# Optimization experiments

Hardware: AMD Instinct MI355X
Metric: run time of the kernel (lower is better)

## Reference

```python
import jax, jax.numpy as jnp
import numpy as np

B, L, ENC = 128, 196, 512
E, D, A, V = 512, 512, 512, 10000
MAXLEN = 26


def setup_inputs() -> dict:
    key = jax.random.key(0)
    ks = jax.random.split(key, 24)
    f32 = jnp.float32
    def rn(k, shape, scale=0.02):
        return jax.random.normal(k, shape, f32) * scale
    lengths = jax.random.randint(ks[2], (B,), 2, MAXLEN + 1).at[0].set(MAXLEN)
    return {
        'encoder_out': jax.random.normal(ks[0], (B, L, ENC), f32),
        'captions': jax.random.randint(ks[1], (B, MAXLEN), 0, V),
        'caption_lengths': lengths,
        # embedding and output layer: uniform(-0.1, 0.1) per _init_weights
        'emb': jax.random.uniform(ks[3], (V, E), f32, -0.1, 0.1),
        'W_ih': rn(ks[4], (E, 4 * D)), 'W_hh': rn(ks[5], (D, 4 * D)),
        'b_lstm': jnp.zeros((4 * D,), f32),
        # sentinel gate of AdaptiveLSTMCell
        'Wx_s': rn(ks[6], (E, D)), 'Wh_s': rn(ks[7], (D, D)), 'b_s': jnp.zeros((D,), f32),
        # adaptive attention MLP
        'W_v': rn(ks[8], (ENC, A)), 'b_v': jnp.zeros((A,), f32),
        'W_g': rn(ks[9], (D, A)), 'b_g': jnp.zeros((A,), f32),
        'W_s_att': rn(ks[10], (ENC, A)), 'b_sa': jnp.zeros((A,), f32),
        'w_a': rn(ks[11], (A,)),
        # hidden-state init layers
        'W_init_h': rn(ks[12], (ENC, D)), 'b_init_h': jnp.zeros((D,), f32),
        'W_init_c': rn(ks[13], (ENC, D)), 'b_init_c': jnp.zeros((D,), f32),
        # deep output layer
        'W_Lh': rn(ks[14], (D, E)), 'b_Lh': jnp.zeros((E,), f32),
        'W_Lz': rn(ks[15], (ENC, E)), 'b_Lz': jnp.zeros((E,), f32),
        'W_Lo': jax.random.uniform(ks[16], (E, V), f32, -0.1, 0.1),
        'b_Lo': jnp.zeros((V,), f32),
    }


def reference(encoder_out, captions, caption_lengths, emb, W_ih, W_hh, b_lstm,
              Wx_s, Wh_s, b_s, W_v, b_v, W_g, b_g, W_s_att, b_sa, w_a,
              W_init_h, b_init_h, W_init_c, b_init_c, W_Lh, b_Lh, W_Lz, b_Lz,
              W_Lo, b_Lo):
    T = captions.shape[1] - 1  # static max decode length (lengths max == MAXLEN)
    mean_ann = encoder_out.mean(axis=1)                       # (B, ENC)
    h0 = jnp.tanh(mean_ann @ W_init_h + b_init_h)             # (B, D)
    c0 = jnp.tanh(mean_ann @ W_init_c + b_init_c)
    att_v = encoder_out @ W_v + b_v                           # (B, L, A), hoisted out of the loop

    def step(carry, words):
        h, c = carry
        x = emb[words]                                        # (B, E) embedding gather
        gates = x @ W_ih + h @ W_hh + b_lstm                  # (B, 4D)
        i, f, g, o = jnp.split(gates, 4, axis=-1)
        c_new = jax.nn.sigmoid(f) * c + jax.nn.sigmoid(i) * jnp.tanh(g)
        h_new = jax.nn.sigmoid(o) * jnp.tanh(c_new)
        s_gate = jax.nn.sigmoid(x @ Wx_s + h @ Wh_s + b_s)    # sentinel (input) gate
        s = s_gate * jnp.tanh(c_new)                          # visual sentinel
        ag = h_new @ W_g + b_g                                # (B, A)
        e_v = jnp.tanh(att_v + ag[:, None, :]) @ w_a          # (B, L)
        e_s = jnp.tanh(s @ W_s_att + b_sa + ag) @ w_a         # (B,)
        a_hat = jax.nn.softmax(jnp.concatenate([e_v, e_s[:, None]], axis=1), axis=1)
        alpha, beta = a_hat[:, :-1], a_hat[:, -1]             # (B,L), (B,)
        ctx = jnp.einsum('bl,ble->be', alpha, encoder_out) + beta[:, None] * s
        logits = (x + h_new @ W_Lh + b_Lh + ctx @ W_Lz + b_Lz) @ W_Lo + b_Lo
        return (h_new, c_new), (logits, alpha, beta)

    words_t = captions[:, :T].T                               # (T, B)
    _, (preds, alphas, betas) = jax.lax.scan(step, (h0, c0), words_t)
    preds = preds.transpose(1, 0, 2)                          # (B, T, V)
    alphas = alphas.transpose(1, 0, 2)                        # (B, T, L)
    betas = betas.T                                           # (B, T)
    dec_len = jnp.clip(caption_lengths - 1, 1)
    active = (jnp.arange(T)[None, :] < dec_len[:, None]).astype(preds.dtype)
    return preds, alphas * active[:, :, None], betas * active
```

## Files before the change

kernel.cpp:

```cpp
#include <hip/hip_runtime.h>
#include <hip/hip_bf16.h>
#include <cstdint>
#include <cstddef>

using bf16 = __hip_bfloat16;
typedef __attribute__((ext_vector_type(4))) float f32x4;
typedef __attribute__((ext_vector_type(8))) short bf16x8;

#define B_ 128
#define L_ 196
#define T_ 25
#define V_ 10000
#define ESCL 2.885390081777927f

__device__ __forceinline__ float b2f(short s) {
  unsigned u = ((unsigned)(unsigned short)s) << 16;
  return __uint_as_float(u);
}
__device__ __forceinline__ bf16 f2b(float f) { return __float2bfloat16(f); }
__device__ __forceinline__ short f2bs(float f) {
  return __builtin_bit_cast(short, __float2bfloat16(f));
}
__device__ __forceinline__ float sigf(float x) { return 1.f / (1.f + __expf(-x)); }
__device__ __forceinline__ float tanh_fast(float x) { return 1.f - 2.f / (1.f + __expf(2.f * x)); }

__device__ __forceinline__ void cst_u32(unsigned* p, unsigned v) {
  __hip_atomic_store(p, v, __ATOMIC_RELAXED, __HIP_MEMORY_SCOPE_AGENT);
}
__device__ __forceinline__ unsigned cld_u32(const unsigned* p) {
  return __hip_atomic_load((unsigned*)p, __ATOMIC_RELAXED, __HIP_MEMORY_SCOPE_AGENT);
}

__device__ __forceinline__ size_t pidx(int row, int col, int K) {
  int KT = K >> 5;
  return (((size_t)(row >> 4) * KT + (col >> 5)) * 64 +
          (size_t)(((col & 31) >> 3) * 16 + (row & 15))) * 8 + (col & 7);
}

__device__ __forceinline__ float wred_sum(float x) {
#pragma unroll
  for (int off = 32; off >= 1; off >>= 1) x += __shfl_xor(x, off, 64);
  return x;
}
__device__ __forceinline__ float wred_max(float x) {
#pragma unroll
  for (int off = 32; off >= 1; off >>= 1) x = fmaxf(x, __shfl_xor(x, off, 64));
  return x;
}

__device__ __forceinline__ void gbar32(unsigned* bs, int mi, int di) {
  asm volatile("s_waitcnt vmcnt(0)" ::: "memory");
  __syncthreads();
  if (threadIdx.x == 0) {
    unsigned* base = bs + mi * 256;
    unsigned* gen  = base + 160;
    unsigned g = cld_u32(gen);
    unsigned a = __hip_atomic_fetch_add(base + (di & 3) * 32, 1u, __ATOMIC_RELAXED,
                                        __HIP_MEMORY_SCOPE_AGENT);
    bool rel = false;
    if ((a & 7u) == 7u) {
      unsigned b = __hip_atomic_fetch_add(base + 128, 1u, __ATOMIC_RELAXED,
                                          __HIP_MEMORY_SCOPE_AGENT);
      if ((b & 3u) == 3u) { cst_u32(gen, g + 1u); rel = true; }
    }
    if (!rel) {
      while (cld_u32(gen) == g) __builtin_amdgcn_s_sleep(1);
    }
  }
  __syncthreads();
}

__global__ __launch_bounds__(256) void scan_ws(
    bf16* __restrict__ hbuf,
    const bf16* __restrict__ WT_gh,
    const bf16* __restrict__ xg,
    float* __restrict__ cbuf,
    bf16* __restrict__ Aag,
    bf16* __restrict__ projA,
    unsigned* __restrict__ bar)
{
  const int tid = threadIdx.x;
  const int wv = tid >> 6, lane = tid & 63;
  const int mi = blockIdx.x >> 5;
  const int di = blockIdx.x & 31;
  __shared__ f32x4 pacc[4][5][64];

  bf16x8 bw[5][4];
#pragma unroll
  for (int g = 0; g < 5; g++)
#pragma unroll
    for (int kk = 0; kk < 4; kk++)
      bw[g][kk] = *(const bf16x8*)(const void*)(
          WT_gh + (size_t)(g * 32 + di) * 8192 + (size_t)(wv * 4 + kk) * 512 + lane * 8);

  const int el_r16 = lane & 15, el_r = lane >> 4;
  const int m_pw = mi * 16 + wv * 4 + el_r;
  const int d_pw = di * 16 + el_r16;
  const size_t qlo = pidx(m_pw, d_pw, 512);
  const size_t plo = pidx(m_pw, d_pw, 1024);
  const size_t phi = pidx(m_pw, 512 + d_pw, 1024);
  float* cp = cbuf + m_pw * 512 + d_pw;

  for (int tt = 0; tt < T_; ++tt) {
    const short* xr = (const short*)(const void*)(
        xg + (size_t)tt * (128 * 2560) + (size_t)m_pw * 2560 + d_pw);
    float xv0 = b2f(xr[0]);
    float xv1 = b2f(xr[512]);
    float xv2 = b2f(xr[1024]);
    float xv3 = b2f(xr[1536]);
    float xv4 = b2f(xr[2048]);
    const bf16* ap = hbuf + (size_t)tt * 65536 + (size_t)mi * 8192 + lane * 8;
    bf16x8 a0 = *(const bf16x8*)(const void*)(ap + (size_t)(wv * 4 + 0) * 512);
    bf16x8 a1 = *(const bf16x8*)(const void*)(ap + (size_t)(wv * 4 + 1) * 512);
    bf16x8 a2 = *(const bf16x8*)(const void*)(ap + (size_t)(wv * 4 + 2) * 512);
    bf16x8 a3 = *(const bf16x8*)(const void*)(ap + (size_t)(wv * 4 + 3) * 512);
    f32x4 acc[5];
#pragma unroll
    for (int g = 0; g < 5; g++) acc[g] = f32x4{0.f, 0.f, 0.f, 0.f};
#pragma unroll
    for (int g = 0; g < 5; g++) {
      acc[g] = __builtin_amdgcn_mfma_f32_16x16x32_bf16(a0, bw[g][0], acc[g], 0, 0, 0);
      acc[g] = __builtin_amdgcn_mfma_f32_16x16x32_bf16(a1, bw[g][1], acc[g], 0, 0, 0);
      acc[g] = __builtin_amdgcn_mfma_f32_16x16x32_bf16(a2, bw[g][2], acc[g], 0, 0, 0);
      acc[g] = __builtin_amdgcn_mfma_f32_16x16x32_bf16(a3, bw[g][3], acc[g], 0, 0, 0);
    }
#pragma unroll
    for (int g = 0; g < 5; g++) pacc[wv][g][lane] = acc[g];
    __syncthreads();
    float G0 = 0.f, G1 = 0.f, G2 = 0.f, G3 = 0.f, G4 = 0.f;
#pragma unroll
    for (int q = 0; q < 4; q++) {
      int sl = wv * 16 + el_r16;
      G0 += pacc[q][0][sl][el_r];
      G1 += pacc[q][1][sl][el_r];
      G2 += pacc[q][2][sl][el_r];
      G3 += pacc[q][3][sl][el_r];
      G4 += pacc[q][4][sl][el_r];
    }
    float cn = sigf(G1 + xv1) * (*cp) + sigf(G0 + xv0) * tanh_fast(G2 + xv2);
    float tcn = tanh_fast(cn);
    float hn = sigf(G3 + xv3) * tcn;
    float ss = sigf(G4 + xv4) * tcn;
    float hn1 = __shfl_down(hn, 1);
    float ss1 = __shfl_down(ss, 1);
    unsigned hp = 0, sp = 0;
    bool wr = !(el_r16 & 1);
    if (wr) {
      hp = (unsigned)(unsigned short)f2bs(hn) |
           ((unsigned)(unsigned short)f2bs(hn1) << 16);
      sp = (unsigned)(unsigned short)f2bs(ss) |
           ((unsigned)(unsigned short)f2bs(ss1) << 16);
      cst_u32((unsigned*)(void*)(hbuf + (size_t)(tt + 1) * 65536 + qlo), hp);
    }
    if (tt < T_ - 1) gbar32(bar, mi, di);
    *cp = cn;
    if (wr) {
      bf16* pA = projA + (size_t)tt * 131072;
      bf16* AagT = Aag + (size_t)tt * 131072;
      *(unsigned*)(void*)(pA + plo) = hp;
      *(unsigned*)(void*)(AagT + plo) = hp;
      *(unsigned*)(void*)(AagT + phi) = sp;
    }
  }
}

__global__ __launch_bounds__(256) void e_batch(
    const bf16* __restrict__ attv, const bf16* __restrict__ agsw_all,
    const float* __restrict__ w_a, const int* __restrict__ clen,
    float* __restrict__ alphas, float* __restrict__ betas,
    float* __restrict__ alphas_raw, float* __restrict__ betas_raw)
{
  __shared__ float sh[200];
  __shared__ float red[8];
  int b = blockIdx.x, t = blockIdx.y;
  int tid = threadIdx.x, wv = tid >> 6, lane = tid & 63;
  const bf16* ag = agsw_all + ((size_t)t * 128 + b) * 1024;
  int a0 = lane * 8;
  float ag8[8], wa8[8], sw8[8];
  float wsum = 0.f;
  bf16x8 agv = *(const bf16x8*)(const void*)(ag + a0);
  bf16x8 swv = *(const bf16x8*)(const void*)(ag + 512 + a0);
#pragma unroll
  for (int j = 0; j < 8; j++) {
    ag8[j] = b2f(agv[j]);
    wa8[j] = w_a[a0 + j];
    sw8[j] = b2f(swv[j]);
    wsum += wa8[j];
  }
  wsum = wred_sum(wsum);
  for (int base = wv; base < 197; base += 16) {
    bf16x8 av[4];
#pragma unroll
    for (int q = 0; q < 4; q++) {
      int l = base + 4 * q;
      if (l < 196)
        av[q] = *(const bf16x8*)(const void*)(attv + ((size_t)(b * 196 + l)) * 512 + a0);
    }
#pragma unroll
    for (int q = 0; q < 4; q++) {
      int l = base + 4 * q;
      if (l > 196) continue;
      float part = 0.f;
      if (l < 196) {
#pragma unroll
        for (int j = 0; j < 8; j++) {
          float z = b2f(av[q][j]) + ag8[j];
          float E = __builtin_amdgcn_exp2f(z);
          part = fmaf(wa8[j], __builtin_amdgcn_rcpf(1.f + E), part);
        }
      } else {
#pragma unroll
        for (int j = 0; j < 8; j++) {
          float z = sw8[j] + ag8[j];
          float E = __builtin_amdgcn_exp2f(z);
          part = fmaf(wa8[j], __builtin_amdgcn_rcpf(1.f + E), part);
        }
      }
      part = wred_sum(part);
      if (lane == 0) sh[l] = wsum - 2.f * part;
    }
  }
  __syncthreads();
  float v = (tid < 197) ? sh[tid] : -1e30f;
  float mx = wred_max(v);
  if (lane == 0) red[wv] = mx;
  __syncthreads();
  mx = fmaxf(fmaxf(red[0], red[1]), fmaxf(red[2], red[3]));
  float p = (tid < 197) ? __expf(v - mx) : 0.f;
  float sm = wred_sum(p);
  if (lane == 0) red[4 + wv] = sm;
  __syncthreads();
  float inv = 1.f / (red[4] + red[5] + red[6] + red[7]);
  float a = p * inv;
  int dec = clen[b] - 1; if (dec < 1) dec = 1;
  float act = (t < dec) ? 1.f : 0.f;
  if (tid < 196) {
    alphas[(size_t)b * (T_ * L_) + (size_t)t * L_ + tid] = a * act;
    alphas_raw[(size_t)b * (T_ * L_) + (size_t)t * L_ + tid] = a;
  }
  if (tid == 196) {
    betas[b * T_ + t] = a * act;
    betas_raw[b * T_ + t] = a;
  }
}

__global__ __launch_bounds__(256) void ctx_tail(
    const float* __restrict__ alphas_raw, const float* __restrict__ betas_raw,
    const bf16* __restrict__ enc_r, const bf16* __restrict__ Aag,
    bf16* __restrict__ projA)
{
  int b = blockIdx.x, cs = blockIdx.y, tid = threadIdx.x;
  __shared__ float al[T_ * 200];
  for (int i = tid; i < T_ * 196; i += 256) {
    al[(i / 196) * 200 + (i % 196)] = alphas_raw[(size_t)b * (T_ * 196) + i];
  }
  __syncthreads();
  int ch = cs * 256 + tid;
  float acc[T_];
#pragma unroll
  for (int t = 0; t < T_; t++) acc[t] = 0.f;
  const short* ep = (const short*)(const void*)(enc_r) + (size_t)b * 196 * 512 + ch;
#pragma unroll 4
  for (int l = 0; l < 196; l++) {
    float e = b2f(ep[(size_t)l * 512]);
#pragma unroll
    for (int t = 0; t < T_; t++) acc[t] += al[t * 200 + l] * e;
  }
#pragma unroll
  for (int t = 0; t < T_; t++) {
    float beta = betas_raw[b * T_ + t];
    float sv = b2f(((const short*)(const void*)Aag)[(size_t)t * 131072 + pidx(b, 512 + ch, 1024)]);
    projA[(size_t)t * 131072 + pidx(b, 512 + ch, 1024)] = f2b(acc[t] + beta * sv);
  }
}

enum { EPI_F32 = 0, EPI_BF16 = 1, EPI_INIT = 2, EPI_PROJ = 3, EPI_OUT = 4 };

template<int MFRAG, int NFRAG, int EPI>
__global__ __launch_bounds__(256) void gemm_pk(
    const bf16* __restrict__ A, const bf16* __restrict__ BT,
    const float* __restrict__ bias, void* __restrict__ Cp,
    const bf16* __restrict__ auxA, float* __restrict__ auxB,
    int M, int N, int K, int ldc, float oscale)
{
  const int lane = threadIdx.x & 63;
  const int wv = threadIdx.x >> 6;
  const int r16 = lane & 15;
  const int kg = lane >> 4;
  const int m0 = blockIdx.x * (MFRAG * 16);
  const int n0 = blockIdx.y * (NFRAG * 64) + wv * (NFRAG * 16);
  const int KT = K >> 5;

  f32x4 acc[MFRAG][NFRAG];
#pragma unroll
  for (int i = 0; i < MFRAG; i++)
#pragma unroll
    for (int j = 0; j < NFRAG; j++) acc[i][j] = f32x4{0.f, 0.f, 0.f, 0.f};

  const bf16* ap = A + (size_t)(m0 >> 4) * KT * 512 + lane * 8;
  const bf16* bp = BT + (size_t)(n0 >> 4) * KT * 512 + lane * 8;

#pragma unroll 4
  for (int kt = 0; kt < KT; kt++) {
    bf16x8 af[MFRAG], bfr[NFRAG];
#pragma unroll
    for (int i = 0; i < MFRAG; i++)
      af[i] = *(const bf16x8*)(const void*)(ap + ((size_t)i * KT + kt) * 512);
#pragma unroll
    for (int j = 0; j < NFRAG; j++)
      bfr[j] = *(const bf16x8*)(const void*)(bp + ((size_t)j * KT + kt) * 512);
#pragma unroll
    for (int i = 0; i < MFRAG; i++)
#pragma unroll
      for (int j = 0; j < NFRAG; j++)
        acc[i][j] = __builtin_amdgcn_mfma_f32_16x16x32_bf16(af[i], bfr[j], acc[i][j], 0, 0, 0);
  }

#pragma unroll
  for (int i = 0; i < MFRAG; i++)
#pragma unroll
    for (int j = 0; j < NFRAG; j++)
#pragma unroll
      for (int r = 0; r < 4; r++) {
        int m = m0 + i * 16 + kg * 4 + r;
        int n = n0 + j * 16 + r16;
        if (n >= N) continue;
        float v = acc[i][j][r] + bias[n];
        if constexpr (EPI == EPI_F32) {
          ((float*)Cp)[(size_t)m * ldc + n] = v * oscale;
        } else if constexpr (EPI == EPI_BF16) {
          ((bf16*)Cp)[(size_t)m * ldc + n] = f2b(v * oscale);
        } else if constexpr (EPI == EPI_INIT) {
          float tv = tanhf(v);
          if (n < 512) ((bf16*)Cp)[pidx(m, n, 512)] = f2b(tv);
          else auxB[(size_t)m * 512 + (n - 512)] = tv;
        } else if constexpr (EPI == EPI_PROJ) {
          v += b2f(((const short*)auxA)[pidx(m, n, 512)]);
          ((bf16*)Cp)[pidx(m, n, 512)] = f2b(v);
        } else {
          int t = m >> 7, b = m & 127;
          ((float*)Cp)[(size_t)b * (T_ * V_) + (size_t)t * V_ + n] = v;
        }
      }
}

#define NJOBS 10
struct TJobs {
  const float* top[NJOBS];
  const float* bot[NJOBS];
  bf16* dst[NJOBS];
  int ncols[NJOBS];
  int ktop[NJOBS];
  int K[NJOBS];
  long cum[NJOBS + 1];
};

__global__ void trans_pack_multi(TJobs J, long total)
{
  for (long u = (long)blockIdx.x * blockDim.x + threadIdx.x; u < total;
       u += (long)gridDim.x * blockDim.x) {
    int j = 0;
#pragma unroll
    for (int q = 1; q < NJOBS; q++) j += (u >= J.cum[q]) ? 1 : 0;
    long t8 = u - J.cum[j];
    int K = J.K[j], KT = K >> 5, ktop = J.ktop[j], ncols = J.ncols[j];
    const float* top = J.top[j];
    const float* bot = J.bot[j];
    int r = (int)(t8 & 15);
    int kg = (int)((t8 >> 4) & 3);
    long tile = t8 >> 6;
    int kt = (int)(tile % KT);
    int rt = (int)(tile / KT);
    int n = rt * 16 + r;
    int kb = kt * 32 + kg * 8;
    bf16x8 out;
#pragma unroll
    for (int jj = 0; jj < 8; jj++) {
      int k = kb + jj;
      float v = 0.f;
      if (n < ncols) {
        if (k < ktop) { if (top) v = top[(size_t)k * ncols + n]; }
        else if (bot) { v = bot[(size_t)(k - ktop) * ncols + n]; }
      }
      out[jj] = f2bs(v);
    }
    *(bf16x8*)(void*)(J.dst[j] + t8 * 8) = out;
  }
}

__global__ void trans_pack(const float* __restrict__ top, const float* __restrict__ bot,
                           bf16* __restrict__ dst, int ncols, long nElem8, int ktop, int K)
{
  int KT = K >> 5;
  for (long t8 = (long)blockIdx.x * blockDim.x + threadIdx.x; t8 < nElem8;
       t8 += (long)gridDim.x * blockDim.x) {
    int r = (int)(t8 & 15);
    int kg = (int)((t8 >> 4) & 3);
    long tile = t8 >> 6;
    int kt = (int)(tile % KT);
    int rt = (int)(tile / KT);
    int n = rt * 16 + r;
    int kb = kt * 32 + kg * 8;
    bf16x8 out;
#pragma unroll
    for (int j = 0; j < 8; j++) {
      int k = kb + j;
      float v = 0.f;
      if (n < ncols) {
        if (k < ktop) { if (top) v = top[(size_t)k * ncols + n]; }
        else if (bot) { v = bot[(size_t)(k - ktop) * ncols + n]; }
      }
      out[j] = f2bs(v);
    }
    *(bf16x8*)(void*)(dst + t8 * 8) = out;
  }
}

__global__ void conv_pack(const float* __restrict__ src, bf16* __restrict__ dst,
                          bf16* __restrict__ dst_row, long nElem8)
{
  for (long t8 = (long)blockIdx.x * blockDim.x + threadIdx.x; t8 < nElem8;
       t8 += (long)gridDim.x * blockDim.x) {
    int r = (int)(t8 & 15);
    int kg = (int)((t8 >> 4) & 3);
    long tile = t8 >> 6;
    int kt = (int)(tile & 15);
    int rt = (int)(tile >> 4);
    size_t rowoff = ((size_t)(rt * 16 + r)) * 512 + kt * 32 + kg * 8;
    const float* s = src + rowoff;
    bf16x8 out;
#pragma unroll
    for (int j = 0; j < 8; j++) out[j] = f2bs(s[j]);
    *(bf16x8*)(void*)(dst + t8 * 8) = out;
    *(bf16x8*)(void*)(dst_row + rowoff) = out;
  }
}

__global__ void bias_comb(const float* __restrict__ b_lstm, const float* __restrict__ b_s,
                          const float* __restrict__ b_g, const float* __restrict__ b_sa,
                          const float* __restrict__ b_Lh, const float* __restrict__ b_Lz,
                          const float* __restrict__ b_ih, const float* __restrict__ b_ic,
                          float* __restrict__ bg, float* __restrict__ ba,
                          float* __restrict__ bp, float* __restrict__ bi)
{
  int i = blockIdx.x * blockDim.x + threadIdx.x;
  if (i < 2560) bg[i] = (i < 2048) ? b_lstm[i] : b_s[i - 2048];
  if (i < 1024) ba[i] = (i < 512) ? b_g[i] : b_sa[i - 512];
  if (i < 512)  bp[i] = b_Lh[i] + b_Lz[i];
  if (i < 1024) bi[i] = (i < 512) ? b_ih[i] : b_ic[i - 512];
}

__global__ __launch_bounds__(128) void mean_enc(const float* __restrict__ enc,
                                                bf16* __restrict__ mb)
{
  int b = blockIdx.x, c = blockIdx.y * 128 + threadIdx.x;
  float s = 0.f;
  for (int l = 0; l < L_; l++) s += enc[((size_t)b * L_ + l) * 512 + c];
  mb[pidx(b, c, 512)] = f2b(s * (1.f / (float)L_));
}

__global__ void gather_x(const float* __restrict__ emb, const int* __restrict__ caps,
                         bf16* __restrict__ xbuf)
{
  int tb = blockIdx.x;
  int t = tb >> 7, b = tb & 127;
  int word = caps[b * 26 + t];
  int c0 = threadIdx.x * 8;
  const float* src = emb + (size_t)word * 512 + c0;
  bf16* dst = xbuf + pidx(tb, c0, 512);
  bf16x8 out;
#pragma unroll
  for (int j = 0; j < 8; j++) out[j] = f2bs(src[j]);
  *(bf16x8*)(void*)dst = out;
}

extern "C" void kernel_launch(void* const* d_in, const int* in_sizes, int n_in,
                              void* d_out, int out_size, void* d_ws, size_t ws_size,
                              hipStream_t stream)
{
  const float* enc      = (const float*)d_in[0];
  const int*   caps     = (const int*)d_in[1];
  const int*   clen     = (const int*)d_in[2];
  const float* emb      = (const float*)d_in[3];
  const float* W_ih     = (const float*)d_in[4];
  const float* W_hh     = (const float*)d_in[5];
  const float* b_lstm   = (const float*)d_in[6];
  const float* Wx_s     = (const float*)d_in[7];
  const float* Wh_s     = (const float*)d_in[8];
  const float* b_s      = (const float*)d_in[9];
  const float* W_v      = (const float*)d_in[10];
  const float* b_v      = (const float*)d_in[11];
  const float* W_g      = (const float*)d_in[12];
  const float* b_g      = (const float*)d_in[13];
  const float* W_s_att  = (const float*)d_in[14];
  const float* b_sa     = (const float*)d_in[15];
  const float* w_a      = (const float*)d_in[16];
  const float* W_init_h = (const float*)d_in[17];
  const float* b_init_h = (const float*)d_in[18];
  const float* W_init_c = (const float*)d_in[19];
  const float* b_init_c = (const float*)d_in[20];
  const float* W_Lh     = (const float*)d_in[21];
  const float* b_Lh     = (const float*)d_in[22];
  const float* W_Lz     = (const float*)d_in[23];
  const float* b_Lz     = (const float*)d_in[24];
  const float* W_Lo     = (const float*)d_in[25];
  const float* b_Lo     = (const float*)d_in[26];

  float* preds  = (float*)d_out;
  float* alphas = preds + (size_t)B_ * T_ * V_;
  float* betas  = alphas + (size_t)B_ * T_ * L_;

  char* ws = (char*)d_ws;
  size_t off = 0;
  auto alloc = [&](size_t bytes) -> void* {
    void* p = ws + off;
    off = (off + bytes + 255) & ~(size_t)255;
    return p;
  };
  bf16*  enc_p  = (bf16*)alloc((size_t)B_ * L_ * 512 * 2);
  bf16*  enc_r  = (bf16*)alloc((size_t)B_ * L_ * 512 * 2);
  bf16*  attv_b = (bf16*)alloc((size_t)B_ * L_ * 512 * 2);
  bf16*  WT_gx  = (bf16*)alloc((size_t)2560 * 512 * 2);
  bf16*  WT_gh  = (bf16*)alloc((size_t)2560 * 512 * 2);
  bf16*  WT_a   = (bf16*)alloc((size_t)1024 * 1024 * 2);
  bf16*  WT_p   = (bf16*)alloc((size_t)512 * 1024 * 2);
  bf16*  WT_v   = (bf16*)alloc((size_t)512 * 512 * 2);
  bf16*  WT_i   = (bf16*)alloc((size_t)1024 * 512 * 2);
  float* bgx    = (float*)alloc(2560 * 4);
  float* bax    = (float*)alloc(1024 * 4);
  float* bpx    = (float*)alloc(512 * 4);
  float* bix    = (float*)alloc(1024 * 4);
  bf16*  mean_b = (bf16*)alloc(128 * 512 * 2);
  bf16*  xbuf   = (bf16*)alloc((size_t)T_ * 128 * 512 * 2);
  bf16*  hbuf   = (bf16*)alloc((size_t)(T_ + 1) * 128 * 512 * 2);
  bf16*  projA  = (bf16*)alloc((size_t)T_ * 128 * 1024 * 2);
  bf16*  agsw_b = (bf16*)alloc((size_t)T_ * 128 * 1024 * 2);
  float* cbuf   = (float*)alloc(128 * 512 * 4);
  unsigned* bar = (unsigned*)alloc(8192);
  if (off > ws_size) return;

  bf16*  xg         = (bf16*)enc_p;
  bf16*  Aag        = (bf16*)((char*)enc_p + 16384000);
  float* alphas_raw = (float*)((char*)enc_p + 22937600);
  float* betas_raw  = (float*)((char*)enc_p + 25446400);
  bf16*  WT_lo = xg;
  bf16*  projb = (bf16*)((char*)xg + 10485760);

  hipMemsetAsync(bar, 0, 8192, stream);

  bias_comb<<<dim3(10), dim3(256), 0, stream>>>(b_lstm, b_s, b_g, b_sa, b_Lh, b_Lz,
                                                b_init_h, b_init_c, bgx, bax, bpx, bix);
  {
    TJobs J;
    auto set = [&](int j, const float* top, const float* bot, bf16* dst,
                   int ncols, int nrows, int ktop, int K) {
      J.top[j] = top; J.bot[j] = bot; J.dst[j] = dst;
      J.ncols[j] = ncols; J.ktop[j] = ktop; J.K[j] = K;
      J.cum[j + 1] = J.cum[j] + (long)nrows * K / 8;
    };
    J.cum[0] = 0;
    set(0, W_ih, nullptr, WT_gx, 2048, 2048, 512, 512);
    set(1, Wx_s, nullptr, WT_gx + (size_t)2048 * 512, 512, 512, 512, 512);
    set(2, W_hh, nullptr, WT_gh, 2048, 2048, 512, 512);
    set(3, Wh_s, nullptr, WT_gh + (size_t)2048 * 512, 512, 512, 512, 512);
    set(4, W_Lh, W_Lz, WT_p, 512, 512, 512, 1024);
    set(5, W_g, nullptr, WT_a, 512, 512, 512, 1024);
    set(6, nullptr, W_s_att, WT_a + (size_t)512 * 1024, 512, 512, 512, 1024);
    set(7, W_v, nullptr, WT_v, 512, 512, 512, 512);
    set(8, W_init_h, nullptr, WT_i, 512, 512, 512, 512);
    set(9, W_init_c, nullptr, WT_i + (size_t)512 * 512, 512, 512, 512, 512);
    long total = J.cum[NJOBS];
    int blocks = (int)((total + 255) / 256);
    if (blocks > 2048) blocks = 2048;
    trans_pack_multi<<<dim3(blocks), dim3(256), 0, stream>>>(J, total);
  }
  conv_pack<<<dim3(4096), dim3(256), 0, stream>>>(enc, enc_p, enc_r,
                                                  (long)B_ * L_ * 512 / 8);
  mean_enc<<<dim3(128, 4), dim3(128), 0, stream>>>(enc, mean_b);
  gather_x<<<dim3(T_ * 128), dim3(64), 0, stream>>>(emb, caps, xbuf);

  gemm_pk<1, 1, EPI_INIT><<<dim3(8, 16), dim3(256), 0, stream>>>(
      mean_b, WT_i, bix, (void*)hbuf, nullptr, cbuf, 128, 1024, 512, 0, 1.f);
  gemm_pk<4, 2, EPI_BF16><<<dim3(392, 4), dim3(256), 0, stream>>>(
      enc_p, WT_v, b_v, attv_b, nullptr, nullptr, B_ * L_, 512, 512, 512, ESCL);
  gemm_pk<4, 2, EPI_BF16><<<dim3(50, 20), dim3(256), 0, stream>>>(
      xbuf, WT_gx, bgx, xg, nullptr, nullptr, T_ * 128, 2560, 512, 2560, 1.f);

  scan_ws<<<dim3(256), dim3(256), 0, stream>>>(hbuf, WT_gh, xg, cbuf, Aag, projA, bar);

  gemm_pk<4, 2, EPI_BF16><<<dim3(50, 8), dim3(256), 0, stream>>>(
      Aag, WT_a, bax, agsw_b, nullptr, nullptr, T_ * 128, 1024, 1024, 1024, ESCL);
  e_batch<<<dim3(128, 25), dim3(256), 0, stream>>>(
      attv_b, agsw_b, w_a, clen, alphas, betas, alphas_raw, betas_raw);
  {
    long n8 = (long)10240 * 512 / 8;
    trans_pack<<<dim3(2048), dim3(256), 0, stream>>>(W_Lo, nullptr, WT_lo,
                                                     10000, n8, 512, 512);
  }
  ctx_tail<<<dim3(128, 2), dim3(256), 0, stream>>>(alphas_raw, betas_raw, enc_r,
                                                   Aag, projA);
  gemm_pk<4, 2, EPI_PROJ><<<dim3(50, 4), dim3(256), 0, stream>>>(
      projA, WT_p, bpx, projb, xbuf, nullptr, T_ * 128, 512, 1024, 0, 1.f);
  gemm_pk<4, 4, EPI_OUT><<<dim3(50, 40), dim3(256), 0, stream>>>(
      projb, WT_lo, b_Lo, preds, nullptr, nullptr, T_ * 128, V_, 512, 0, 1.f);
}
```

Baseline: 440.7 us.

## Use tanh addition identity in attention scoring and enlarge GEMM M tiles

Attention scoring now uses the identity tanh(a+b) = (ta+tb)/(1+ta*tb). The att_v and ag/sentinel GEMM epilogues store tanh values, so the per-element inner loop in e_batch drops the exp2 and keeps only a reciprocal and some FMAs. Separately, several GEMM launches double MFRAG from 4 to 8 and halve the grid in M, which raises per-block reuse. The identity introduces bf16 rounding on the tanh operands, which may cost accuracy. The larger tiles raise register pressure and cut the number of blocks.

```diff
diff --git a/kernel.cpp b/kernel.cpp
--- a/kernel.cpp
+++ b/kernel.cpp
@@ -11,7 +11,6 @@
 #define L_ 196
 #define T_ 25
 #define V_ 10000
-#define ESCL 2.885390081777927f
 
 __device__ __forceinline__ float b2f(short s) {
   unsigned u = ((unsigned)(unsigned short)s) << 16;
@@ -177,7 +176,6 @@
   const bf16* ag = agsw_all + ((size_t)t * 128 + b) * 1024;
   int a0 = lane * 8;
   float ag8[8], wa8[8], sw8[8];
-  float wsum = 0.f;
   bf16x8 agv = *(const bf16x8*)(const void*)(ag + a0);
   bf16x8 swv = *(const bf16x8*)(const void*)(ag + 512 + a0);
 #pragma unroll
@@ -185,9 +183,7 @@
     ag8[j] = b2f(agv[j]);
     wa8[j] = w_a[a0 + j];
     sw8[j] = b2f(swv[j]);
-    wsum += wa8[j];
-  }
-  wsum = wred_sum(wsum);
+  }
   for (int base = wv; base < 197; base += 16) {
     bf16x8 av[4];
 #pragma unroll
@@ -204,20 +200,22 @@
       if (l < 196) {
 #pragma unroll
         for (int j = 0; j < 8; j++) {
-          float z = b2f(av[q][j]) + ag8[j];
-          float E = __builtin_amdgcn_exp2f(z);
-          part = fmaf(wa8[j], __builtin_amdgcn_rcpf(1.f + E), part);
+          float Ta = b2f(av[q][j]);
+          float den = fmaf(Ta, ag8[j], 1.f);
+          float num = Ta + ag8[j];
+          part = fmaf(num * __builtin_amdgcn_rcpf(den), wa8[j], part);
         }
       } else {
 #pragma unroll
         for (int j = 0; j < 8; j++) {
-          float z = sw8[j] + ag8[j];
-          float E = __builtin_amdgcn_exp2f(z);
-          part = fmaf(wa8[j], __builtin_amdgcn_rcpf(1.f + E), part);
+          float Ta = sw8[j];
+          float den = fmaf(Ta, ag8[j], 1.f);
+          float num = Ta + ag8[j];
+          part = fmaf(num * __builtin_amdgcn_rcpf(den), wa8[j], part);
         }
       }
       part = wred_sum(part);
-      if (lane == 0) sh[l] = wsum - 2.f * part;
+      if (lane == 0) sh[l] = part;
     }
   }
   __syncthreads();
@@ -274,7 +272,7 @@
   }
 }
 
-enum { EPI_F32 = 0, EPI_BF16 = 1, EPI_INIT = 2, EPI_PROJ = 3, EPI_OUT = 4 };
+enum { EPI_F32 = 0, EPI_BF16 = 1, EPI_INIT = 2, EPI_PROJ = 3, EPI_OUT = 4, EPI_TANH = 5 };
 
 template<int MFRAG, int NFRAG, int EPI>
 __global__ __launch_bounds__(256) void gemm_pk(
@@ -330,6 +328,8 @@
           ((float*)Cp)[(size_t)m * ldc + n] = v * oscale;
         } else if constexpr (EPI == EPI_BF16) {
           ((bf16*)Cp)[(size_t)m * ldc + n] = f2b(v * oscale);
+        } else if constexpr (EPI == EPI_TANH) {
+          ((bf16*)Cp)[(size_t)m * ldc + n] = f2b(tanh_fast(v));
         } else if constexpr (EPI == EPI_INIT) {
           float tv = tanhf(v);
           if (n < 512) ((bf16*)Cp)[pidx(m, n, 512)] = f2b(tv);
@@ -581,15 +581,15 @@
 
   gemm_pk<1, 1, EPI_INIT><<<dim3(8, 16), dim3(256), 0, stream>>>(
       mean_b, WT_i, bix, (void*)hbuf, nullptr, cbuf, 128, 1024, 512, 0, 1.f);
-  gemm_pk<4, 2, EPI_BF16><<<dim3(392, 4), dim3(256), 0, stream>>>(
-      enc_p, WT_v, b_v, attv_b, nullptr, nullptr, B_ * L_, 512, 512, 512, ESCL);
-  gemm_pk<4, 2, EPI_BF16><<<dim3(50, 20), dim3(256), 0, stream>>>(
+  gemm_pk<8, 2, EPI_TANH><<<dim3(196, 4), dim3(256), 0, stream>>>(
+      enc_p, WT_v, b_v, attv_b, nullptr, nullptr, B_ * L_, 512, 512, 512, 1.f);
+  gemm_pk<8, 2, EPI_BF16><<<dim3(25, 20), dim3(256), 0, stream>>>(
       xbuf, WT_gx, bgx, xg, nullptr, nullptr, T_ * 128, 2560, 512, 2560, 1.f);
 
   scan_ws<<<dim3(256), dim3(256), 0, stream>>>(hbuf, WT_gh, xg, cbuf, Aag, projA, bar);
 
-  gemm_pk<4, 2, EPI_BF16><<<dim3(50, 8), dim3(256), 0, stream>>>(
-      Aag, WT_a, bax, agsw_b, nullptr, nullptr, T_ * 128, 1024, 1024, 1024, ESCL);
+  gemm_pk<8, 2, EPI_TANH><<<dim3(25, 8), dim3(256), 0, stream>>>(
+      Aag, WT_a, bax, agsw_b, nullptr, nullptr, T_ * 128, 1024, 1024, 1024, 1.f);
   e_batch<<<dim3(128, 25), dim3(256), 0, stream>>>(
       attv_b, agsw_b, w_a, clen, alphas, betas, alphas_raw, betas_raw);
   {
@@ -601,6 +601,6 @@
                                                    Aag, projA);
   gemm_pk<4, 2, EPI_PROJ><<<dim3(50, 4), dim3(256), 0, stream>>>(
       projA, WT_p, bpx, projb, xbuf, nullptr, T_ * 128, 512, 1024, 0, 1.f);
-  gemm_pk<4, 4, EPI_OUT><<<dim3(50, 40), dim3(256), 0, stream>>>(
+  gemm_pk<8, 4, EPI_OUT><<<dim3(25, 40), dim3(256), 0, stream>>>(
       projb, WT_lo, b_Lo, preds, nullptr, nullptr, T_ * 128, V_, 512, 0, 1.f);
 }
```

New measurement: 467.4 us. +6.0%, slower.
